# Kernel tuning notes

Measured on AMD Instinct MI355X. Metric: run time of the kernel, lower is better.

Reference implementation:

```python
import jax, jax.numpy as jnp
import numpy as np

K_INIT = 16  # self.k from __init__

def setup_inputs() -> dict:
    key = jax.random.key(0)
    center = jax.random.normal(key, (8192, 64), dtype=jnp.float32)
    return {"center": center}

def _cdist(x):
    # Euclidean pairwise distances, matmul-based like torch.cdist(p=2).
    x2 = jnp.sum(x * x, axis=-1)  # [N]
    d2 = x2[:, None] + x2[None, :] - 2.0 * (x @ x.T)  # [N, N]
    d2 = jnp.maximum(d2, 0.0)
    # safe sqrt (grad-safe at 0; forward identical)
    d = jnp.sqrt(jnp.where(d2 > 0.0, d2, 1.0))
    return jnp.where(d2 > 0.0, d, 0.0)

def reference(center):
    n, d_feat = center.shape
    k = min(K_INIT + 1, d_feat)  # faithful to torch: min(self.k + 1, center.shape[1])
    dist = _cdist(center)  # [N, N]
    # smallest-k via top_k on negated distances
    _, indices = jax.lax.top_k(-dist, k)  # [N, k]
    neighbor_indices = indices[:, 1:]  # drop self, [N, k-1]
    mean_dists = jnp.take_along_axis(dist, neighbor_indices, axis=1).mean(axis=1)  # [N]
    logp = jax.nn.log_softmax(mean_dists, axis=0)  # = softmax(mean_dists).log()
    q = 1.0 / n
    # F.kl_div(p.log(), q, reduction='sum') = sum q * (log q - log p)
    loss = jnp.sum(q * (jnp.log(jnp.float32(q)) - logp))
    return loss
```

## Files before the change

kernel.cpp:

```cpp
#include <hip/hip_runtime.h>
#include <hip/hip_bf16.h>
#include <math.h>

#define N_PTS 8192
#define D_FEAT 64
#define TPB 1024
#define ROWS_B 32
#define PASSES 16
#define RSTR 648
#define LSTR 20

typedef __attribute__((ext_vector_type(8))) short short8v;
typedef __attribute__((ext_vector_type(16))) float f32x16;

__device__ ushort g_X2[N_PTS * D_FEAT];
__device__ float  g_x2n[N_PTS];
__device__ float  g_md[N_PTS];

__global__ __launch_bounds__(256) void pack_kernel(const float* __restrict__ x) {
    const int row = blockIdx.x * 256 + threadIdx.x;
    const int chunk = row >> 5, r = row & 31;
    const float4* xr = (const float4*)(x + (size_t)row * D_FEAT);
    ushort* base = g_X2 + (size_t)chunk * 2048 + r * 8;
    float norm = 0.f;
    #pragma unroll
    for (int it = 0; it < 8; ++it) {
        float4 a = xr[2 * it], b = xr[2 * it + 1];
        float vals[8] = {a.x, a.y, a.z, a.w, b.x, b.y, b.z, b.w};
        uint hi[8];
        #pragma unroll
        for (int e = 0; e < 8; ++e) {
            float v = vals[e];
            norm += v * v;
            uint u = __float_as_uint(v);
            hi[e] = (u + 0x7fffu + ((u >> 16) & 1u)) >> 16;
        }
        *(uint4*)(base + it * 256) = make_uint4(
            hi[0] | (hi[1] << 16), hi[2] | (hi[3] << 16),
            hi[4] | (hi[5] << 16), hi[6] | (hi[7] << 16));
    }
    g_x2n[row] = norm;
}

#define CE(A, B) { float lo_ = fminf(A, B); float hi_ = fmaxf(A, B); A = lo_; B = hi_; }

__global__ __launch_bounds__(TPB, 4) void nn_kernel() {
    __shared__ float s_mem[32 * RSTR];
    const int t    = threadIdx.x;
    const int lane = t & 63;
    const int w    = t >> 6;
    const int il   = lane & 31;
    const int h    = lane >> 5;
    const int ib   = blockIdx.x;
    const int i0   = ib * ROWS_B;
    const float INF = __builtin_inff();

    {
        float4* s4 = (float4*)s_mem;
        const float4* g4 = (const float4*)g_x2n;
        #pragma unroll
        for (int q = 0; q < 2; ++q) s4[t + q * TPB] = g4[t + q * TPB];
    }

    const short8v* Xf = (const short8v*)g_X2;

    short8v bfr[4];
    {
        const short8v* bp = Xf + ((size_t)ib * 8 + h) * 32 + il;
        #pragma unroll
        for (int tt = 0; tt < 4; ++tt) bfr[tt] = bp[tt * 64];
    }
    __syncthreads();

    float t16[16];
    #pragma unroll
    for (int k = 0; k < 16; ++k) t16[k] = INF;

    const short8v* abase = Xf + ((size_t)w * 8 + h) * 32 + il;
    #define ALOAD(dst, p) { \
        const short8v* ab_ = abase + (size_t)(p) * 4096; \
        _Pragma("unroll") \
        for (int tt = 0; tt < 4; ++tt) dst[tt] = ab_[tt * 64]; }

    #define EPILOG(accv, p) { \
        const int cl_ = (p) * 16 + w; \
        float c[16]; \
        _Pragma("unroll") \
        for (int g = 0; g < 4; ++g) { \
            float4 xq = *(const float4*)&s_mem[cl_ * 32 + 8 * g + 4 * h]; \
            float cand[4] = {xq.x, xq.y, xq.z, xq.w}; \
            _Pragma("unroll") \
            for (int e = 0; e < 4; ++e) \
                c[4 * g + e] = fmaf(-2.f, accv[4 * g + e], cand[e]); \
        } \
         \
        CE(c[0],c[8]) CE(c[1],c[9]) CE(c[2],c[10]) CE(c[3],c[11]) \
        CE(c[4],c[12]) CE(c[5],c[13]) CE(c[6],c[14]) CE(c[7],c[15]) \
        CE(c[0],c[4]) CE(c[1],c[5]) CE(c[2],c[6]) CE(c[3],c[7]) \
        CE(c[8],c[12]) CE(c[9],c[13]) CE(c[10],c[14]) CE(c[11],c[15]) \
        CE(c[4],c[8]) CE(c[5],c[9]) CE(c[6],c[10]) CE(c[7],c[11]) \
        CE(c[0],c[2]) CE(c[1],c[3]) CE(c[4],c[6]) CE(c[5],c[7]) \
        CE(c[8],c[10]) CE(c[9],c[11]) CE(c[12],c[14]) CE(c[13],c[15]) \
        CE(c[2],c[8]) CE(c[3],c[9]) CE(c[6],c[12]) CE(c[7],c[13]) \
        CE(c[2],c[4]) CE(c[3],c[5]) CE(c[6],c[8]) CE(c[7],c[9]) \
        CE(c[10],c[12]) CE(c[11],c[13]) \
        CE(c[0],c[1]) CE(c[2],c[3]) CE(c[4],c[5]) CE(c[6],c[7]) \
        CE(c[8],c[9]) CE(c[10],c[11]) CE(c[12],c[13]) CE(c[14],c[15]) \
        CE(c[1],c[8]) CE(c[3],c[10]) CE(c[5],c[12]) CE(c[7],c[14]) \
        CE(c[1],c[4]) CE(c[3],c[6]) CE(c[5],c[8]) CE(c[7],c[10]) \
        CE(c[9],c[12]) CE(c[11],c[14]) \
        CE(c[1],c[2]) CE(c[3],c[4]) CE(c[5],c[6]) CE(c[7],c[8]) \
        CE(c[9],c[10]) CE(c[11],c[12]) CE(c[13],c[14]) \
         \
        _Pragma("unroll") \
        for (int i = 0; i < 16; ++i) t16[i] = fminf(t16[i], c[15 - i]); \
        _Pragma("unroll") \
        for (int j = 8; j > 0; j >>= 1) { \
            _Pragma("unroll") \
            for (int i = 0; i < 16; ++i) { \
                const int ix = i ^ j; \
                if (ix > i) { \
                    float lo = fminf(t16[i], t16[ix]); \
                    float hi = fmaxf(t16[i], t16[ix]); \
                    t16[i] = lo; \
                    t16[ix] = hi; \
                } \
            } \
        } }

    #define MFMA4(accv, areg) { \
        _Pragma("unroll") \
        for (int r = 0; r < 16; ++r) accv[r] = 0.f; \
        _Pragma("unroll") \
        for (int tt = 0; tt < 4; ++tt) \
            accv = __builtin_amdgcn_mfma_f32_32x32x16_bf16(areg[tt], bfr[tt], accv, 0, 0, 0); }

    short8v a0[4], a1[4];
    f32x16 acc;
    ALOAD(a0, 0);
    #pragma unroll 1
    for (int pp = 0; pp < PASSES / 2; ++pp) {
        const int p0 = 2 * pp, p1 = 2 * pp + 1;
        ALOAD(a1, p1);
        MFMA4(acc, a0);
        EPILOG(acc, p0);
        if (pp < PASSES / 2 - 1) ALOAD(a0, p0 + 2);
        MFMA4(acc, a1);
        EPILOG(acc, p1);
    }

    {
        const bool own = (w == (ib & 15)) && (h == ((il >> 2) & 1));
        if (own) {
            #pragma unroll
            for (int k = 0; k < 15; ++k) t16[k] = t16[k + 1];
            t16[15] = INF;
        }
    }

    __syncthreads();
    {
        const int list = w * 2 + h;
        float* dst = &s_mem[il * RSTR + list * LSTR];
        *(float4*)(dst + 0)  = make_float4(t16[0],  t16[1],  t16[2],  t16[3]);
        *(float4*)(dst + 4)  = make_float4(t16[4],  t16[5],  t16[6],  t16[7]);
        *(float4*)(dst + 8)  = make_float4(t16[8],  t16[9],  t16[10], t16[11]);
        *(float4*)(dst + 12) = make_float4(t16[12], t16[13], t16[14], t16[15]);
    }
    __syncthreads();

    {
        const int q  = lane >> 5;
        const int sl = lane & 31;
        const int r  = w * 2 + q;
        const int row = i0 + r;
        float tl[16];
        {
            const float* src = &s_mem[r * RSTR + sl * LSTR];
            float4 q0 = *(const float4*)(src + 0);
            float4 q1 = *(const float4*)(src + 4);
            float4 q2 = *(const float4*)(src + 8);
            float4 q3 = *(const float4*)(src + 12);
            tl[0]=q0.x; tl[1]=q0.y; tl[2]=q0.z; tl[3]=q0.w;
            tl[4]=q1.x; tl[5]=q1.y; tl[6]=q1.z; tl[7]=q1.w;
            tl[8]=q2.x; tl[9]=q2.y; tl[10]=q2.z; tl[11]=q2.w;
            tl[12]=q3.x; tl[13]=q3.y; tl[14]=q3.z; tl[15]=q3.w;
        }
        const float x2r = g_x2n[row];
        float sum = 0.f;
        #pragma unroll 1
        for (int it = 0; it < 16; ++it) {
            float m = tl[0]; int src = sl;
            #pragma unroll
            for (int off = 16; off > 0; off >>= 1) {
                float om = __shfl_xor(m, off);
                int os = __shfl_xor(src, off);
                if (om < m || (om == m && os < src)) { m = om; src = os; }
            }
            sum += sqrtf(fmaxf(m + x2r, 0.f));
            const bool pop = (sl == src);
            #pragma unroll
            for (int k = 0; k < 15; ++k) tl[k] = pop ? tl[k + 1] : tl[k];
            tl[15] = pop ? INF : tl[15];
        }
        if (sl == 0) g_md[row] = sum * (1.f / 16.f);
    }
}

__global__ __launch_bounds__(1024) void loss_kernel(float* __restrict__ out) {
    __shared__ float s[1024];
    const int t = threadIdx.x;

    float m = -__builtin_inff();
    for (int j = t; j < N_PTS; j += 1024) m = fmaxf(m, g_md[j]);
    s[t] = m; __syncthreads();
    for (int off = 512; off > 0; off >>= 1) {
        if (t < off) s[t] = fmaxf(s[t], s[t + off]);
        __syncthreads();
    }
    m = s[0]; __syncthreads();

    float se = 0.f, sm = 0.f;
    for (int j = t; j < N_PTS; j += 1024) {
        float v = g_md[j];
        se += expf(v - m);
        sm += v;
    }
    s[t] = se; __syncthreads();
    for (int off = 512; off > 0; off >>= 1) {
        if (t < off) s[t] += s[t + off];
        __syncthreads();
    }
    float S = s[0]; __syncthreads();
    s[t] = sm; __syncthreads();
    for (int off = 512; off > 0; off >>= 1) {
        if (t < off) s[t] += s[t + off];
        __syncthreads();
    }
    float M = s[0];

    if (t == 0) {
        const float n = (float)N_PTS;
        out[0] = -logf(n) - M / n + (m + logf(S));
    }
}

extern "C" void kernel_launch(void* const* d_in, const int* in_sizes, int n_in,
                              void* d_out, int out_size, void* d_ws, size_t ws_size,
                              hipStream_t stream) {
    const float* x = (const float*)d_in[0];
    float* out = (float*)d_out;

    pack_kernel<<<N_PTS / 256, 256, 0, stream>>>(x);
    nn_kernel<<<N_PTS / ROWS_B, TPB, 0, stream>>>();
    loss_kernel<<<1, 1024, 0, stream>>>(out);
}
```

Before: 56.02 us.

## Replace per-lane top-16 sorting with two-pass threshold filter and compaction

The previous kernel kept a sorted top-16 list per lane and merged sorted candidates every pass. The new version runs the MFMA distance computation twice. The first pass tracks one per-lane minimum, and a bitonic sort across 32 lanes turns those into a threshold equal to the 17th smallest lane minimum. The second pass appends every candidate at or below that threshold to a per-row LDS buffer through shared atomics, then sorts and merges that buffer to take the 17 smallest, dropping the self entry. This removes the heavy per-pass sorting network at the cost of doubling the GEMM work and LDS atomics. Correctness depends on the candidate count per row staying within a cap of 512, so rows with many candidates near the threshold would be silently truncated.

```diff
diff --git a/kernel.cpp b/kernel.cpp
--- a/kernel.cpp
+++ b/kernel.cpp
@@ -7,8 +7,12 @@
 #define TPB 1024
 #define ROWS_B 32
 #define PASSES 16
-#define RSTR 648
-#define LSTR 20
+#define CAP 512
+#define NORM_OFF 0
+#define MIN_OFF  8192
+#define TAU_OFF  9216
+#define SV_OFF   9248
+#define LDS_F    (9248 + 32 * CAP)
 
 typedef __attribute__((ext_vector_type(8))) short short8v;
 typedef __attribute__((ext_vector_type(16))) float f32x16;
@@ -45,7 +49,8 @@
 #define CE(A, B) { float lo_ = fminf(A, B); float hi_ = fmaxf(A, B); A = lo_; B = hi_; }
 
 __global__ __launch_bounds__(TPB, 4) void nn_kernel() {
-    __shared__ float s_mem[32 * RSTR];
+    __shared__ float s_mem[LDS_F];
+    __shared__ int   s_cnt[32];
     const int t    = threadIdx.x;
     const int lane = t & 63;
     const int w    = t >> 6;
@@ -60,6 +65,7 @@
         const float4* g4 = (const float4*)g_x2n;
         #pragma unroll
         for (int q = 0; q < 2; ++q) s4[t + q * TPB] = g4[t + q * TPB];
+        if (t < 32) s_cnt[t] = 0;
     }
 
     const short8v* Xf = (const short8v*)g_X2;
@@ -71,10 +77,6 @@
         for (int tt = 0; tt < 4; ++tt) bfr[tt] = bp[tt * 64];
     }
     __syncthreads();
-
-    float t16[16];
-    #pragma unroll
-    for (int k = 0; k < 16; ++k) t16[k] = INF;
 
     const short8v* abase = Xf + ((size_t)w * 8 + h) * 32 + il;
     #define ALOAD(dst, p) { \
@@ -82,114 +84,130 @@
         _Pragma("unroll") \
         for (int tt = 0; tt < 4; ++tt) dst[tt] = ab_[tt * 64]; }
 
-    #define EPILOG(accv, p) { \
+    #define MFMA4(accv, areg) { \
+        _Pragma("unroll") \
+        for (int r = 0; r < 16; ++r) accv[r] = 0.f; \
+        _Pragma("unroll") \
+        for (int tt = 0; tt < 4; ++tt) \
+            accv = __builtin_amdgcn_mfma_f32_32x32x16_bf16(areg[tt], bfr[tt], accv, 0, 0, 0); }
+
+    float mmin = INF;
+    #define EPILOG_MIN(accv, p) { \
         const int cl_ = (p) * 16 + w; \
-        float c[16]; \
         _Pragma("unroll") \
         for (int g = 0; g < 4; ++g) { \
             float4 xq = *(const float4*)&s_mem[cl_ * 32 + 8 * g + 4 * h]; \
             float cand[4] = {xq.x, xq.y, xq.z, xq.w}; \
             _Pragma("unroll") \
             for (int e = 0; e < 4; ++e) \
-                c[4 * g + e] = fmaf(-2.f, accv[4 * g + e], cand[e]); \
-        } \
-         \
-        CE(c[0],c[8]) CE(c[1],c[9]) CE(c[2],c[10]) CE(c[3],c[11]) \
-        CE(c[4],c[12]) CE(c[5],c[13]) CE(c[6],c[14]) CE(c[7],c[15]) \
-        CE(c[0],c[4]) CE(c[1],c[5]) CE(c[2],c[6]) CE(c[3],c[7]) \
-        CE(c[8],c[12]) CE(c[9],c[13]) CE(c[10],c[14]) CE(c[11],c[15]) \
-        CE(c[4],c[8]) CE(c[5],c[9]) CE(c[6],c[10]) CE(c[7],c[11]) \
-        CE(c[0],c[2]) CE(c[1],c[3]) CE(c[4],c[6]) CE(c[5],c[7]) \
-        CE(c[8],c[10]) CE(c[9],c[11]) CE(c[12],c[14]) CE(c[13],c[15]) \
-        CE(c[2],c[8]) CE(c[3],c[9]) CE(c[6],c[12]) CE(c[7],c[13]) \
-        CE(c[2],c[4]) CE(c[3],c[5]) CE(c[6],c[8]) CE(c[7],c[9]) \
-        CE(c[10],c[12]) CE(c[11],c[13]) \
-        CE(c[0],c[1]) CE(c[2],c[3]) CE(c[4],c[5]) CE(c[6],c[7]) \
-        CE(c[8],c[9]) CE(c[10],c[11]) CE(c[12],c[13]) CE(c[14],c[15]) \
-        CE(c[1],c[8]) CE(c[3],c[10]) CE(c[5],c[12]) CE(c[7],c[14]) \
-        CE(c[1],c[4]) CE(c[3],c[6]) CE(c[5],c[8]) CE(c[7],c[10]) \
-        CE(c[9],c[12]) CE(c[11],c[14]) \
-        CE(c[1],c[2]) CE(c[3],c[4]) CE(c[5],c[6]) CE(c[7],c[8]) \
-        CE(c[9],c[10]) CE(c[11],c[12]) CE(c[13],c[14]) \
-         \
-        _Pragma("unroll") \
-        for (int i = 0; i < 16; ++i) t16[i] = fminf(t16[i], c[15 - i]); \
-        _Pragma("unroll") \
-        for (int j = 8; j > 0; j >>= 1) { \
+                mmin = fminf(mmin, fmaf(-2.f, accv[4 * g + e], cand[e])); \
+        } }
+
+    {
+        short8v a0[4], a1[4];
+        f32x16 acc;
+        ALOAD(a0, 0);
+        #pragma unroll 1
+        for (int pp = 0; pp < PASSES / 2; ++pp) {
+            const int p0 = 2 * pp, p1 = 2 * pp + 1;
+            ALOAD(a1, p1);
+            MFMA4(acc, a0);
+            EPILOG_MIN(acc, p0);
+            if (pp < PASSES / 2 - 1) ALOAD(a0, p0 + 2);
+            MFMA4(acc, a1);
+            EPILOG_MIN(acc, p1);
+        }
+    }
+    s_mem[MIN_OFF + il * 32 + (w * 2 + h)] = mmin;
+    __syncthreads();
+
+    {
+        const int r2 = 2 * w + (lane >> 5);
+        const int idx = lane & 31;
+        float m = s_mem[MIN_OFF + r2 * 32 + idx];
+        #pragma unroll
+        for (int k = 2; k <= 32; k <<= 1) {
+            #pragma unroll
+            for (int j = k >> 1; j > 0; j >>= 1) {
+                float o = __shfl_xor(m, j);
+                const bool low = ((idx & j) == 0);
+                const bool up  = ((idx & k) == 0);
+                float mn = fminf(m, o), mx = fmaxf(m, o);
+                m = (low == up) ? mn : mx;
+            }
+        }
+        if (idx == 16) s_mem[TAU_OFF + r2] = m;
+    }
+    __syncthreads();
+
+    const float mytau = s_mem[TAU_OFF + il];
+    #define EPILOG_FLT(accv, p) { \
+        const int cl_ = (p) * 16 + w; \
+        _Pragma("unroll") \
+        for (int g = 0; g < 4; ++g) { \
+            float4 xq = *(const float4*)&s_mem[cl_ * 32 + 8 * g + 4 * h]; \
+            float cand[4] = {xq.x, xq.y, xq.z, xq.w}; \
             _Pragma("unroll") \
-            for (int i = 0; i < 16; ++i) { \
-                const int ix = i ^ j; \
-                if (ix > i) { \
-                    float lo = fminf(t16[i], t16[ix]); \
-                    float hi = fmaxf(t16[i], t16[ix]); \
-                    t16[i] = lo; \
-                    t16[ix] = hi; \
+            for (int e = 0; e < 4; ++e) { \
+                float v = fmaf(-2.f, accv[4 * g + e], cand[e]); \
+                if (v <= mytau) { \
+                    int ix_ = atomicAdd(&s_cnt[il], 1); \
+                    if (ix_ < CAP) s_mem[SV_OFF + il * CAP + ix_] = v; \
                 } \
             } \
         } }
 
-    #define MFMA4(accv, areg) { \
-        _Pragma("unroll") \
-        for (int r = 0; r < 16; ++r) accv[r] = 0.f; \
-        _Pragma("unroll") \
-        for (int tt = 0; tt < 4; ++tt) \
-            accv = __builtin_amdgcn_mfma_f32_32x32x16_bf16(areg[tt], bfr[tt], accv, 0, 0, 0); }
-
-    short8v a0[4], a1[4];
-    f32x16 acc;
-    ALOAD(a0, 0);
-    #pragma unroll 1
-    for (int pp = 0; pp < PASSES / 2; ++pp) {
-        const int p0 = 2 * pp, p1 = 2 * pp + 1;
-        ALOAD(a1, p1);
-        MFMA4(acc, a0);
-        EPILOG(acc, p0);
-        if (pp < PASSES / 2 - 1) ALOAD(a0, p0 + 2);
-        MFMA4(acc, a1);
-        EPILOG(acc, p1);
-    }
-
-    {
-        const bool own = (w == (ib & 15)) && (h == ((il >> 2) & 1));
-        if (own) {
-            #pragma unroll
-            for (int k = 0; k < 15; ++k) t16[k] = t16[k + 1];
-            t16[15] = INF;
-        }
-    }
-
-    __syncthreads();
-    {
-        const int list = w * 2 + h;
-        float* dst = &s_mem[il * RSTR + list * LSTR];
-        *(float4*)(dst + 0)  = make_float4(t16[0],  t16[1],  t16[2],  t16[3]);
-        *(float4*)(dst + 4)  = make_float4(t16[4],  t16[5],  t16[6],  t16[7]);
-        *(float4*)(dst + 8)  = make_float4(t16[8],  t16[9],  t16[10], t16[11]);
-        *(float4*)(dst + 12) = make_float4(t16[12], t16[13], t16[14], t16[15]);
-    }
-    __syncthreads();
-
-    {
-        const int q  = lane >> 5;
+    {
+        short8v a0[4], a1[4];
+        f32x16 acc;
+        ALOAD(a0, 0);
+        #pragma unroll 1
+        for (int pp = 0; pp < PASSES / 2; ++pp) {
+            const int p0 = 2 * pp, p1 = 2 * pp + 1;
+            ALOAD(a1, p1);
+            MFMA4(acc, a0);
+            EPILOG_FLT(acc, p0);
+            if (pp < PASSES / 2 - 1) ALOAD(a0, p0 + 2);
+            MFMA4(acc, a1);
+            EPILOG_FLT(acc, p1);
+        }
+    }
+    __syncthreads();
+
+    {
+        const int r2 = 2 * w + (lane >> 5);
         const int sl = lane & 31;
-        const int r  = w * 2 + q;
-        const int row = i0 + r;
+        const int row = i0 + r2;
+        int n = s_cnt[r2];
+        if (n > CAP) n = CAP;
         float tl[16];
-        {
-            const float* src = &s_mem[r * RSTR + sl * LSTR];
-            float4 q0 = *(const float4*)(src + 0);
-            float4 q1 = *(const float4*)(src + 4);
-            float4 q2 = *(const float4*)(src + 8);
-            float4 q3 = *(const float4*)(src + 12);
-            tl[0]=q0.x; tl[1]=q0.y; tl[2]=q0.z; tl[3]=q0.w;
-            tl[4]=q1.x; tl[5]=q1.y; tl[6]=q1.z; tl[7]=q1.w;
-            tl[8]=q2.x; tl[9]=q2.y; tl[10]=q2.z; tl[11]=q2.w;
-            tl[12]=q3.x; tl[13]=q3.y; tl[14]=q3.z; tl[15]=q3.w;
-        }
+        #pragma unroll
+        for (int q = 0; q < 16; ++q) {
+            const int ix = sl + 32 * q;
+            tl[q] = (ix < n) ? s_mem[SV_OFF + r2 * CAP + ix] : INF;
+        }
+        CE(tl[0],tl[8]) CE(tl[1],tl[9]) CE(tl[2],tl[10]) CE(tl[3],tl[11])
+        CE(tl[4],tl[12]) CE(tl[5],tl[13]) CE(tl[6],tl[14]) CE(tl[7],tl[15])
+        CE(tl[0],tl[4]) CE(tl[1],tl[5]) CE(tl[2],tl[6]) CE(tl[3],tl[7])
+        CE(tl[8],tl[12]) CE(tl[9],tl[13]) CE(tl[10],tl[14]) CE(tl[11],tl[15])
+        CE(tl[4],tl[8]) CE(tl[5],tl[9]) CE(tl[6],tl[10]) CE(tl[7],tl[11])
+        CE(tl[0],tl[2]) CE(tl[1],tl[3]) CE(tl[4],tl[6]) CE(tl[5],tl[7])
+        CE(tl[8],tl[10]) CE(tl[9],tl[11]) CE(tl[12],tl[14]) CE(tl[13],tl[15])
+        CE(tl[2],tl[8]) CE(tl[3],tl[9]) CE(tl[6],tl[12]) CE(tl[7],tl[13])
+        CE(tl[2],tl[4]) CE(tl[3],tl[5]) CE(tl[6],tl[8]) CE(tl[7],tl[9])
+        CE(tl[10],tl[12]) CE(tl[11],tl[13])
+        CE(tl[0],tl[1]) CE(tl[2],tl[3]) CE(tl[4],tl[5]) CE(tl[6],tl[7])
+        CE(tl[8],tl[9]) CE(tl[10],tl[11]) CE(tl[12],tl[13]) CE(tl[14],tl[15])
+        CE(tl[1],tl[8]) CE(tl[3],tl[10]) CE(tl[5],tl[12]) CE(tl[7],tl[14])
+        CE(tl[1],tl[4]) CE(tl[3],tl[6]) CE(tl[5],tl[8]) CE(tl[7],tl[10])
+        CE(tl[9],tl[12]) CE(tl[11],tl[14])
+        CE(tl[1],tl[2]) CE(tl[3],tl[4]) CE(tl[5],tl[6]) CE(tl[7],tl[8])
+        CE(tl[9],tl[10]) CE(tl[11],tl[12]) CE(tl[13],tl[14])
+
         const float x2r = g_x2n[row];
         float sum = 0.f;
         #pragma unroll 1
-        for (int it = 0; it < 16; ++it) {
+        for (int it = 0; it < 17; ++it) {
             float m = tl[0]; int src = sl;
             #pragma unroll
             for (int off = 16; off > 0; off >>= 1) {
@@ -197,7 +215,7 @@
                 int os = __shfl_xor(src, off);
                 if (om < m || (om == m && os < src)) { m = om; src = os; }
             }
-            sum += sqrtf(fmaxf(m + x2r, 0.f));
+            if (it > 0) sum += sqrtf(fmaxf(m + x2r, 0.f));
             const bool pop = (sl == src);
             #pragma unroll
             for (int k = 0; k < 15; ++k) tl[k] = pop ? tl[k + 1] : tl[k];
```

Result: no change. 56.57 us (+1.0%).
